# Kernel optimization log

Measured on AMD Instinct MI355X. Metric: run time of the kernel, lower is better.

Reference implementation:

```python
import jax, jax.numpy as jnp
import numpy as np

N = 8192
DIMS = 128
HID = 64
NEG = -9e15


def setup_inputs() -> dict:
    key = jax.random.key(0)
    k_adj, k_h, k_w1, k_w2 = jax.random.split(key, 4)
    graph_info = (jax.random.uniform(k_adj, (N, N)) < 0.01).astype(jnp.float32)
    h = jax.random.normal(k_h, (N, DIMS), dtype=jnp.float32)
    # xavier-normal-ish init for the 2-layer scoring MLP (dims -> 64 -> 1)
    W1 = jax.random.normal(k_w1, (DIMS, HID), dtype=jnp.float32) * np.sqrt(2.0 / (DIMS + HID))
    b1 = jnp.zeros((HID,), dtype=jnp.float32)
    W2 = jax.random.normal(k_w2, (HID, 1), dtype=jnp.float32) * np.sqrt(2.0 / (HID + 1))
    b2 = jnp.zeros((1,), dtype=jnp.float32)
    return {"graph_info": graph_info, "h": h, "W1": W1, "b1": b1, "W2": W2, "b2": b2}


def reference(graph_info, h, W1, b1, W2, b2):
    # per-node MLP score: e_j for every node j  -> [N, 1]
    e = jnp.dot(jnp.maximum(jnp.dot(h, W1) + b1, 0.0), W2) + b2
    # e.transpose().repeat(N,1): row i sees scores of all columns j -> broadcast [1, N]
    scores = e[:, 0][None, :]
    # mask non-edges with large negative, softmax over neighbors (dim=-1)
    att = jnp.where(graph_info > 0, scores, jnp.float32(NEG))
    att = jax.nn.softmax(att, axis=-1)
    out = jnp.dot(att, h)  # [N, dims] aggregation
    # sum_flag == 1: rescale each row by its degree (diagflat(num) @ h)
    num = jnp.sum(graph_info, axis=-1)  # [N]
    out = num[:, None] * out
    return out
```

## Files before the change

### kernel.cpp

```cpp
#include <hip/hip_runtime.h>
#include <math.h>

#define NN 8192
#define DIMS 128
#define HID 64
#define CAP 192

typedef float f4v __attribute__((ext_vector_type(4)));
typedef float f2v __attribute__((ext_vector_type(2)));

__global__ __launch_bounds__(256) void score_kernel(
    const float* __restrict__ h, const float* __restrict__ W1,
    const float* __restrict__ b1, const float* __restrict__ W2,
    const float* __restrict__ b2, float* __restrict__ ee) {
  __shared__ float sW1[DIMS * HID];
  for (int i = threadIdx.x * 4; i < DIMS * HID; i += 1024)
    *(float4*)&sW1[i] = *(const float4*)&W1[i];
  __syncthreads();
  int wv = threadIdx.x >> 6, lane = threadIdx.x & 63;
  int j0 = blockIdx.x * 16 + wv * 4;
  const float* h0 = h + (size_t)j0 * DIMS;
  float bb = b1[lane];
  float a0 = bb, a1 = bb, a2 = bb, a3 = bb;
#pragma unroll 4
  for (int d = 0; d < DIMS; ++d) {
    float wc = sW1[d * HID + lane];
    a0 = fmaf(h0[d], wc, a0);
    a1 = fmaf(h0[d + DIMS], wc, a1);
    a2 = fmaf(h0[d + 2 * DIMS], wc, a2);
    a3 = fmaf(h0[d + 3 * DIMS], wc, a3);
  }
  float w2 = W2[lane];
  float r0 = fmaxf(a0, 0.f) * w2, r1 = fmaxf(a1, 0.f) * w2;
  float r2 = fmaxf(a2, 0.f) * w2, r3 = fmaxf(a3, 0.f) * w2;
#pragma unroll
  for (int off = 32; off > 0; off >>= 1) {
    r0 += __shfl_xor(r0, off, 64);
    r1 += __shfl_xor(r1, off, 64);
    r2 += __shfl_xor(r2, off, 64);
    r3 += __shfl_xor(r3, off, 64);
  }
  if (lane == 0) {
    float bo = b2[0];
    ee[j0]     = expf(r0 + bo);
    ee[j0 + 1] = expf(r1 + bo);
    ee[j0 + 2] = expf(r2 + bo);
    ee[j0 + 3] = expf(r3 + bo);
  }
}

#define PROC(v, it)                                                                      \
  do {                                                                                   \
    int col = ((it) * 64 + lane) * 4;                                                    \
    unsigned long long m0 = __ballot(v.x > 0.f);                                         \
    unsigned long long m1 = __ballot(v.y > 0.f);                                         \
    unsigned long long m2 = __ballot(v.z > 0.f);                                         \
    unsigned long long m3 = __ballot(v.w > 0.f);                                         \
    if (v.x > 0.f) { int o = cnt + __popcll(m0 & lt); if (o < CAP) rowidx[o] = (unsigned short)col; }       \
    cnt += (int)__popcll(m0);                                                            \
    if (v.y > 0.f) { int o = cnt + __popcll(m1 & lt); if (o < CAP) rowidx[o] = (unsigned short)(col + 1); } \
    cnt += (int)__popcll(m1);                                                            \
    if (v.z > 0.f) { int o = cnt + __popcll(m2 & lt); if (o < CAP) rowidx[o] = (unsigned short)(col + 2); } \
    cnt += (int)__popcll(m2);                                                            \
    if (v.w > 0.f) { int o = cnt + __popcll(m3 & lt); if (o < CAP) rowidx[o] = (unsigned short)(col + 3); } \
    cnt += (int)__popcll(m3);                                                            \
  } while (0)

__global__ __launch_bounds__(256) void compact_kernel(
    const float* __restrict__ graph, unsigned short* __restrict__ idx16,
    int* __restrict__ counts) {
  int w = threadIdx.x >> 6;
  int lane = threadIdx.x & 63;
  int row = blockIdx.x * 4 + w;
  const f4v* g4 = (const f4v*)(graph + (size_t)row * NN);
  unsigned short* rowidx = idx16 + (size_t)row * CAP;
  unsigned long long lt = (1ull << lane) - 1ull;
  int cnt = 0;

  f4v c0 = __builtin_nontemporal_load(g4 + 0 * 64 + lane);
  f4v c1 = __builtin_nontemporal_load(g4 + 1 * 64 + lane);
  f4v c2 = __builtin_nontemporal_load(g4 + 2 * 64 + lane);
  f4v c3 = __builtin_nontemporal_load(g4 + 3 * 64 + lane);
#pragma unroll 1
  for (int it4 = 0; it4 < 8; ++it4) {
    f4v n0, n1, n2, n3;
    if (it4 < 7) {
      const f4v* nb = g4 + (it4 * 4 + 4) * 64 + lane;
      n0 = __builtin_nontemporal_load(nb);
      n1 = __builtin_nontemporal_load(nb + 64);
      n2 = __builtin_nontemporal_load(nb + 128);
      n3 = __builtin_nontemporal_load(nb + 192);
    } else {
      n0 = n1 = n2 = n3 = (f4v)(0.f);
    }
    PROC(c0, it4 * 4 + 0);
    PROC(c1, it4 * 4 + 1);
    PROC(c2, it4 * 4 + 2);
    PROC(c3, it4 * 4 + 3);
    c0 = n0; c1 = n1; c2 = n2; c3 = n3;
  }
  if (lane == 0) counts[row] = cnt < CAP ? cnt : CAP;
}

#define HLD(wj) (*(const float2*)(hbase + ((size_t)__float_as_int((wj).y)) * DIMS))

__global__ __launch_bounds__(256) void gather_kernel(
    const unsigned short* __restrict__ idx16, const int* __restrict__ counts,
    const float* __restrict__ ee, const float* __restrict__ h,
    float* __restrict__ out) {
  __shared__ float2 s_wj[4][CAP];
  int w = threadIdx.x >> 6;
  int lane = threadIdx.x & 63;
  int row = blockIdx.x * 4 + w;
  int count = counts[row];
  const unsigned short* rowidx = idx16 + (size_t)row * CAP;

  float z = 0.f;
  for (int q = lane; q < count; q += 64) {
    int j = rowidx[q];
    float wv = ee[j];
    s_wj[w][q] = make_float2(wv, __int_as_float(j));
    z += wv;
  }
#pragma unroll
  for (int off = 32; off > 0; off >>= 1) z += __shfl_xor(z, off, 64);

  float ax = 0.f, ay = 0.f;
  const float* hbase = h + lane * 2;
  int q = 0;
  int n8 = count & ~7;
  for (; q < n8; q += 8) {
    float2 wj0 = s_wj[w][q + 0], wj1 = s_wj[w][q + 1];
    float2 wj2 = s_wj[w][q + 2], wj3 = s_wj[w][q + 3];
    float2 wj4 = s_wj[w][q + 4], wj5 = s_wj[w][q + 5];
    float2 wj6 = s_wj[w][q + 6], wj7 = s_wj[w][q + 7];
    float2 h0 = HLD(wj0), h1 = HLD(wj1), h2 = HLD(wj2), h3 = HLD(wj3);
    float2 h4 = HLD(wj4), h5 = HLD(wj5), h6 = HLD(wj6), h7 = HLD(wj7);
    ax = fmaf(wj0.x, h0.x, ax); ay = fmaf(wj0.x, h0.y, ay);
    ax = fmaf(wj1.x, h1.x, ax); ay = fmaf(wj1.x, h1.y, ay);
    ax = fmaf(wj2.x, h2.x, ax); ay = fmaf(wj2.x, h2.y, ay);
    ax = fmaf(wj3.x, h3.x, ax); ay = fmaf(wj3.x, h3.y, ay);
    ax = fmaf(wj4.x, h4.x, ax); ay = fmaf(wj4.x, h4.y, ay);
    ax = fmaf(wj5.x, h5.x, ax); ay = fmaf(wj5.x, h5.y, ay);
    ax = fmaf(wj6.x, h6.x, ax); ay = fmaf(wj6.x, h6.y, ay);
    ax = fmaf(wj7.x, h7.x, ax); ay = fmaf(wj7.x, h7.y, ay);
  }
  for (; q < count; ++q) {
    float2 wj = s_wj[w][q];
    float2 hv = HLD(wj);
    ax = fmaf(wj.x, hv.x, ax);
    ay = fmaf(wj.x, hv.y, ay);
  }
  float scale = (count > 0) ? ((float)count / z) : 0.f;
  f2v o2;
  o2.x = ax * scale;
  o2.y = ay * scale;
  __builtin_nontemporal_store(o2, (f2v*)(out + (size_t)row * DIMS + lane * 2));
}

extern "C" void kernel_launch(void* const* d_in, const int* in_sizes, int n_in,
                              void* d_out, int out_size, void* d_ws, size_t ws_size,
                              hipStream_t stream) {
  const float* graph = (const float*)d_in[0];
  const float* h     = (const float*)d_in[1];
  const float* W1    = (const float*)d_in[2];
  const float* b1    = (const float*)d_in[3];
  const float* W2    = (const float*)d_in[4];
  const float* b2    = (const float*)d_in[5];
  float* out = (float*)d_out;

  float* ee = (float*)d_ws;
  int* counts = (int*)((char*)d_ws + NN * sizeof(float));
  unsigned short* idx16 = (unsigned short*)((char*)d_ws + NN * (sizeof(float) + sizeof(int)));

  score_kernel<<<NN / 16, 256, 0, stream>>>(h, W1, b1, W2, b2, ee);
  compact_kernel<<<NN / 4, 256, 0, stream>>>(graph, idx16, counts);
  gather_kernel<<<NN / 4, 256, 0, stream>>>(idx16, counts, ee, h, out);
}
```

Measured before the change: 88.99 us.

## Interleave compaction chunks across waves with atomic row counters; vectorize score loads

The compact kernel now gives each wave 32 chunks of 1 KB spread across the whole adjacency matrix, with a stride of 8192 chunks, instead of one full contiguous row. Per-row output slots are reserved with an atomicAdd on a counts array that score_kernel zeroes beforehand. The goal is to spread concurrent reads over DRAM more evenly. The cost is that neighbor order in each row becomes nondeterministic, so float summation order changes, and one atomic is added per chunk. Nontemporal loads are replaced with plain loads, and score_kernel reads h as float4.

Result: slower. 114.0 us (+28.1%).

```diff
diff --git a/kernel.cpp b/kernel.cpp
--- a/kernel.cpp
+++ b/kernel.cpp
@@ -12,23 +12,29 @@
 __global__ __launch_bounds__(256) void score_kernel(
     const float* __restrict__ h, const float* __restrict__ W1,
     const float* __restrict__ b1, const float* __restrict__ W2,
-    const float* __restrict__ b2, float* __restrict__ ee) {
+    const float* __restrict__ b2, float* __restrict__ ee,
+    int* __restrict__ counts) {
+  if (blockIdx.x < 32) counts[blockIdx.x * 256 + threadIdx.x] = 0;
   __shared__ float sW1[DIMS * HID];
   for (int i = threadIdx.x * 4; i < DIMS * HID; i += 1024)
     *(float4*)&sW1[i] = *(const float4*)&W1[i];
   __syncthreads();
   int wv = threadIdx.x >> 6, lane = threadIdx.x & 63;
   int j0 = blockIdx.x * 16 + wv * 4;
-  const float* h0 = h + (size_t)j0 * DIMS;
+  const f4v* h4 = (const f4v*)(h + (size_t)j0 * DIMS);
   float bb = b1[lane];
   float a0 = bb, a1 = bb, a2 = bb, a3 = bb;
-#pragma unroll 4
-  for (int d = 0; d < DIMS; ++d) {
-    float wc = sW1[d * HID + lane];
-    a0 = fmaf(h0[d], wc, a0);
-    a1 = fmaf(h0[d + DIMS], wc, a1);
-    a2 = fmaf(h0[d + 2 * DIMS], wc, a2);
-    a3 = fmaf(h0[d + 3 * DIMS], wc, a3);
+#pragma unroll 8
+  for (int d4 = 0; d4 < 32; ++d4) {
+    f4v v0 = h4[d4], v1 = h4[d4 + 32], v2 = h4[d4 + 64], v3 = h4[d4 + 96];
+    float w0 = sW1[(d4 * 4 + 0) * HID + lane];
+    float w1 = sW1[(d4 * 4 + 1) * HID + lane];
+    float w2c = sW1[(d4 * 4 + 2) * HID + lane];
+    float w3 = sW1[(d4 * 4 + 3) * HID + lane];
+    a0 = fmaf(v0.x, w0, a0); a0 = fmaf(v0.y, w1, a0); a0 = fmaf(v0.z, w2c, a0); a0 = fmaf(v0.w, w3, a0);
+    a1 = fmaf(v1.x, w0, a1); a1 = fmaf(v1.y, w1, a1); a1 = fmaf(v1.z, w2c, a1); a1 = fmaf(v1.w, w3, a1);
+    a2 = fmaf(v2.x, w0, a2); a2 = fmaf(v2.y, w1, a2); a2 = fmaf(v2.z, w2c, a2); a2 = fmaf(v2.w, w3, a2);
+    a3 = fmaf(v3.x, w0, a3); a3 = fmaf(v3.y, w1, a3); a3 = fmaf(v3.z, w2c, a3); a3 = fmaf(v3.w, w3, a3);
   }
   float w2 = W2[lane];
   float r0 = fmaxf(a0, 0.f) * w2, r1 = fmaxf(a1, 0.f) * w2;
@@ -49,57 +55,62 @@
   }
 }
 
-#define PROC(v, it)                                                                      \
-  do {                                                                                   \
-    int col = ((it) * 64 + lane) * 4;                                                    \
-    unsigned long long m0 = __ballot(v.x > 0.f);                                         \
-    unsigned long long m1 = __ballot(v.y > 0.f);                                         \
-    unsigned long long m2 = __ballot(v.z > 0.f);                                         \
-    unsigned long long m3 = __ballot(v.w > 0.f);                                         \
-    if (v.x > 0.f) { int o = cnt + __popcll(m0 & lt); if (o < CAP) rowidx[o] = (unsigned short)col; }       \
-    cnt += (int)__popcll(m0);                                                            \
-    if (v.y > 0.f) { int o = cnt + __popcll(m1 & lt); if (o < CAP) rowidx[o] = (unsigned short)(col + 1); } \
-    cnt += (int)__popcll(m1);                                                            \
-    if (v.z > 0.f) { int o = cnt + __popcll(m2 & lt); if (o < CAP) rowidx[o] = (unsigned short)(col + 2); } \
-    cnt += (int)__popcll(m2);                                                            \
-    if (v.w > 0.f) { int o = cnt + __popcll(m3 & lt); if (o < CAP) rowidx[o] = (unsigned short)(col + 3); } \
-    cnt += (int)__popcll(m3);                                                            \
+#define PROCQ(v, i)                                                            \
+  do {                                                                         \
+    int chunk = wave_g + (i) * 8192;                                           \
+    int row = chunk >> 5;                                                      \
+    int colbase = (chunk & 31) << 8;                                           \
+    unsigned long long m0 = __ballot(v.x > 0.f);                               \
+    unsigned long long m1 = __ballot(v.y > 0.f);                               \
+    unsigned long long m2 = __ballot(v.z > 0.f);                               \
+    unsigned long long m3 = __ballot(v.w > 0.f);                               \
+    int p0 = (int)__popcll(m0), p1 = (int)__popcll(m1);                        \
+    int p2 = (int)__popcll(m2), p3 = (int)__popcll(m3);                        \
+    int tot = p0 + p1 + p2 + p3;                                               \
+    int base = 0;                                                              \
+    if (lane == 0 && tot > 0) base = atomicAdd(counts + row, tot);             \
+    base = __shfl(base, 0, 64);                                                \
+    unsigned short* rp = idx16 + (size_t)row * CAP;                            \
+    int col = colbase + lane * 4;                                              \
+    int o;                                                                     \
+    o = base + (int)__popcll(m0 & lt);                                         \
+    if (v.x > 0.f && o < CAP) rp[o] = (unsigned short)col;                     \
+    o = base + p0 + (int)__popcll(m1 & lt);                                    \
+    if (v.y > 0.f && o < CAP) rp[o] = (unsigned short)(col + 1);               \
+    o = base + p0 + p1 + (int)__popcll(m2 & lt);                               \
+    if (v.z > 0.f && o < CAP) rp[o] = (unsigned short)(col + 2);               \
+    o = base + p0 + p1 + p2 + (int)__popcll(m3 & lt);                          \
+    if (v.w > 0.f && o < CAP) rp[o] = (unsigned short)(col + 3);               \
   } while (0)
+
+#define CADDR(i) (g4 + ((size_t)(wave_g + (i) * 8192) * 64 + lane))
 
 __global__ __launch_bounds__(256) void compact_kernel(
     const float* __restrict__ graph, unsigned short* __restrict__ idx16,
     int* __restrict__ counts) {
-  int w = threadIdx.x >> 6;
+  int wave_g = (blockIdx.x << 2) + (threadIdx.x >> 6);
   int lane = threadIdx.x & 63;
-  int row = blockIdx.x * 4 + w;
-  const f4v* g4 = (const f4v*)(graph + (size_t)row * NN);
-  unsigned short* rowidx = idx16 + (size_t)row * CAP;
   unsigned long long lt = (1ull << lane) - 1ull;
-  int cnt = 0;
+  const f4v* g4 = (const f4v*)graph;
 
-  f4v c0 = __builtin_nontemporal_load(g4 + 0 * 64 + lane);
-  f4v c1 = __builtin_nontemporal_load(g4 + 1 * 64 + lane);
-  f4v c2 = __builtin_nontemporal_load(g4 + 2 * 64 + lane);
-  f4v c3 = __builtin_nontemporal_load(g4 + 3 * 64 + lane);
+  f4v c0 = *CADDR(0), c1 = *CADDR(1), c2 = *CADDR(2), c3 = *CADDR(3);
 #pragma unroll 1
-  for (int it4 = 0; it4 < 8; ++it4) {
+  for (int t = 0; t < 8; ++t) {
     f4v n0, n1, n2, n3;
-    if (it4 < 7) {
-      const f4v* nb = g4 + (it4 * 4 + 4) * 64 + lane;
-      n0 = __builtin_nontemporal_load(nb);
-      n1 = __builtin_nontemporal_load(nb + 64);
-      n2 = __builtin_nontemporal_load(nb + 128);
-      n3 = __builtin_nontemporal_load(nb + 192);
+    if (t < 7) {
+      n0 = *CADDR(t * 4 + 4);
+      n1 = *CADDR(t * 4 + 5);
+      n2 = *CADDR(t * 4 + 6);
+      n3 = *CADDR(t * 4 + 7);
     } else {
       n0 = n1 = n2 = n3 = (f4v)(0.f);
     }
-    PROC(c0, it4 * 4 + 0);
-    PROC(c1, it4 * 4 + 1);
-    PROC(c2, it4 * 4 + 2);
-    PROC(c3, it4 * 4 + 3);
+    PROCQ(c0, t * 4 + 0);
+    PROCQ(c1, t * 4 + 1);
+    PROCQ(c2, t * 4 + 2);
+    PROCQ(c3, t * 4 + 3);
     c0 = n0; c1 = n1; c2 = n2; c3 = n3;
   }
-  if (lane == 0) counts[row] = cnt < CAP ? cnt : CAP;
 }
 
 #define HLD(wj) (*(const float2*)(hbase + ((size_t)__float_as_int((wj).y)) * DIMS))
@@ -113,6 +124,7 @@
   int lane = threadIdx.x & 63;
   int row = blockIdx.x * 4 + w;
   int count = counts[row];
+  count = count < CAP ? count : CAP;
   const unsigned short* rowidx = idx16 + (size_t)row * CAP;
 
   float z = 0.f;
@@ -173,7 +185,7 @@
   int* counts = (int*)((char*)d_ws + NN * sizeof(float));
   unsigned short* idx16 = (unsigned short*)((char*)d_ws + NN * (sizeof(float) + sizeof(int)));
 
-  score_kernel<<<NN / 16, 256, 0, stream>>>(h, W1, b1, W2, b2, ee);
+  score_kernel<<<NN / 16, 256, 0, stream>>>(h, W1, b1, W2, b2, ee, counts);
   compact_kernel<<<NN / 4, 256, 0, stream>>>(graph, idx16, counts);
   gather_kernel<<<NN / 4, 256, 0, stream>>>(idx16, counts, ee, h, out);
 }
```
